# Optimization experiments

Measured on AMD Instinct MI355X. Metric: run time of the kernel, lower is better.

## Reference

```python
import jax, jax.numpy as jnp
import numpy as np

OIM_SCALAR = 30.0
NUM_PIDS = 5000      # rows of lut_instance
NUM_SAMPLES = 5000   # rows of reid_lut / len(reid_labels) (must equal NUM_PIDS, see source indexing)
NUM_FEATURES = 256
B_TOTAL = 4096       # total RoIs across the image batch
IGNORE_INDEX = 5554


def _l2norm(x):
    return x / jnp.linalg.norm(x, axis=-1, keepdims=True)


def setup_inputs() -> dict:
    key = jax.random.key(0)
    k1, k2, k3, k4, k5 = jax.random.split(key, 5)
    inputs = _l2norm(jax.random.normal(k1, (B_TOTAL, NUM_FEATURES), dtype=jnp.float32))
    # roi_label in [0, NUM_PIDS]; 0 = background (-> target -1, filtered out)
    roi_label = jax.random.randint(k2, (B_TOTAL,), 0, NUM_PIDS + 1, dtype=jnp.int32)
    lut_instance = _l2norm(jax.random.normal(k3, (NUM_PIDS, NUM_FEATURES), dtype=jnp.float32))
    reid_lut = _l2norm(jax.random.normal(k4, (NUM_SAMPLES, NUM_FEATURES), dtype=jnp.float32))
    # per-pid reid class id; -1 = unlabeled instance (filtered by label_reid >= 0)
    reid_labels = jax.random.randint(k5, (NUM_SAMPLES,), 0, NUM_SAMPLES, dtype=jnp.int32) - 1
    return {"inputs": inputs, "roi_label": roi_label, "lut_instance": lut_instance,
            "reid_lut": reid_lut, "reid_labels": reid_labels}


def _forward(inputs, lut_instance, reid_lut, roi_label, reid_labels):
    feat_dim = inputs.shape[1]
    targets = roi_label - 1
    valid = targets >= 0                       # torch: inds = targets >= 0 (masked mean == subset mean)
    label = jnp.clip(targets, 0)
    re_id_features = lut_instance[label]       # [B, F]
    label_reid = reid_labels[label]            # [B]

    w1 = valid.astype(inputs.dtype)
    n1 = jnp.maximum(w1.sum(), 1.0)
    # nn.MSELoss(): mean over all elements of the selected rows
    feature_consistency = jnp.sum(((re_id_features - inputs) ** 2) * w1[:, None]) / (n1 * feat_dim)

    valid2 = valid & (label_reid >= 0)
    w2 = valid2.astype(inputs.dtype)
    n2 = jnp.maximum(w2.sum(), 1.0)
    lr = jnp.clip(label_reid, 0)

    # ---- criterion_instance, vectorized over the double python loop ----
    out_inst = (inputs @ lut_instance.T) * OIM_SCALAR          # [B, P]
    pos_mask = reid_labels[None, :] == label_reid[:, None]     # [B, P] label-equality groups
    neg_logits = jnp.where(pos_mask, -jnp.inf, out_inst)
    lse_neg = jax.scipy.special.logsumexp(neg_logits, axis=1)  # [B]
    # per positive p: -log_softmax over cat([out[k,p]], out[k, negs])[0]
    per_pos = jnp.logaddexp(out_inst, lse_neg[:, None]) - out_inst  # [B, P]
    pos_count = jnp.maximum(pos_mask.sum(axis=1), 1).astype(inputs.dtype)
    loss_k = jnp.sum(jnp.where(pos_mask, per_pos, 0.0), axis=1) / pos_count
    instance_loss = jnp.sum(loss_k * w2) / n2                  # mean over valid reid rows

    # ---- OIM cross entropy against reid_lut ----
    out_reid = (inputs @ reid_lut.T) * OIM_SCALAR              # [B, S]
    logp = jax.nn.log_softmax(out_reid, axis=1)
    ce = -jnp.take_along_axis(logp, lr[:, None], axis=1)[:, 0]
    w3 = w2 * (lr != IGNORE_INDEX).astype(inputs.dtype)
    n3 = jnp.maximum(w3.sum(), 1.0)
    loss_oim_reid = jnp.sum(ce * w3) / n3

    return feature_consistency + loss_oim_reid + instance_loss


def reference(inputs, roi_label, lut_instance, reid_lut, reid_labels):
    return _forward(inputs, lut_instance, reid_lut, roi_label, reid_labels)
```

## Files before the change

### kernel.cpp

```cpp
#include <hip/hip_runtime.h>


#define BT 4096
#define NPID 5000
#define FDIM 256
#define NCHUNK 8
#define BPROWS 10240
#define SIDE 5120
#define SCALE2 43.2808512266689f
#define LN2 0.6931471805599453f
#define PADMARK ((int)0x80000000)
#define FXS 67108864.0

typedef __attribute__((ext_vector_type(8))) _Float16 half8;
typedef __attribute__((ext_vector_type(4))) float f32x4;

#if __has_builtin(__builtin_amdgcn_exp2f)
#define EXP2R(x) __builtin_amdgcn_exp2f(x)
#else
#define EXP2R(x) exp2f(x)
#endif

__device__ __forceinline__ size_t frag_unit(int row, int oct) {
  int c  = oct >> 2;
  int ko = oct & 3;
  return ((size_t)(row >> 4) * NCHUNK + c) * 64 + (row & 15) + (ko << 4);
}

__global__ __launch_bounds__(256) void prep(const float* __restrict__ inputs,
                                            const int* __restrict__ roi,
                                            const float* __restrict__ lut,
                                            const float* __restrict__ reid,
                                            const int* __restrict__ rlab,
                                            _Float16* __restrict__ Ap,
                                            _Float16* __restrict__ Bp,
                                            int* __restrict__ g, int* __restrict__ lr,
                                            float* __restrict__ w2f, float* __restrict__ v1f,
                                            float* __restrict__ fcv,
                                            int* __restrict__ poscnt,
                                            unsigned long long* __restrict__ ctrl) {
  const int b = blockIdx.x, tid = threadIdx.x;
  if (b < 512) {
    int idx = b * 256 + tid;
    int row = idx >> 5, oct = idx & 31;
    const float4* s4 = (const float4*)(inputs + (size_t)row * FDIM + oct * 8);
    float4 f0 = s4[0], f1 = s4[1];
    float fv[8] = {f0.x, f0.y, f0.z, f0.w, f1.x, f1.y, f1.z, f1.w};
    half8 ov;
#pragma unroll
    for (int j = 0; j < 8; ++j) ov[j] = (_Float16)(fv[j] * SCALE2);
    *(half8*)(Ap + frag_unit(row, oct) * 8) = ov;
  } else if (b < 1792) {
    int idx = (b - 512) * 256 + tid;
    int row = idx >> 5, oct = idx & 31;
    const float* src = nullptr;
    if (row < NPID) src = lut + (size_t)row * FDIM + oct * 8;
    else if (row >= SIDE && row < SIDE + NPID) src = reid + (size_t)(row - SIDE) * FDIM + oct * 8;
    half8 ov;
    if (src) {
      const float4* s4 = (const float4*)src;
      float4 f0 = s4[0], f1 = s4[1];
      float fv[8] = {f0.x, f0.y, f0.z, f0.w, f1.x, f1.y, f1.z, f1.w};
#pragma unroll
      for (int j = 0; j < 8; ++j) ov[j] = (_Float16)fv[j];
    } else {
#pragma unroll
      for (int j = 0; j < 8; ++j) ov[j] = (_Float16)0.f;
    }
    *(half8*)(Bp + frag_unit(row, oct) * 8) = ov;
  } else if (b < 2816) {
    int gt = (b - 1792) * 256 + tid;
    int row = gt >> 6, lane = gt & 63;
    int t = roi[row] - 1;
    bool valid = t >= 0;
    int label = t > 0 ? t : 0;
    int gg = rlab[label];
    const float4* xv = (const float4*)(inputs + (size_t)row * FDIM);
    const float4* lv = (const float4*)(lut + (size_t)label * FDIM);
    float4 a = xv[lane], bb = lv[lane];
    float dx = bb.x - a.x, dy = bb.y - a.y, dz = bb.z - a.z, dw = bb.w - a.w;
    float s = dx * dx + dy * dy + dz * dz + dw * dw;
#pragma unroll
    for (int d = 1; d < 64; d <<= 1) s += __shfl_xor(s, d, 64);
    if (lane == 0) {
      g[row]   = gg;
      lr[row]  = gg > 0 ? gg : 0;
      w2f[row] = (valid && gg >= 0) ? 1.0f : 0.0f;
      v1f[row] = valid ? 1.0f : 0.0f;
      fcv[row] = valid ? s : 0.0f;
    }
  } else {
    int idx = (b - 2816) * 256 + tid;
    poscnt[idx] = 0;
    if (b == 2816 && tid < 8) ctrl[tid] = 0ULL;
  }
}

__global__ __launch_bounds__(256, 3) void gemm_main(const _Float16* __restrict__ Ap,
                                                    const _Float16* __restrict__ Bp,
                                                    const int* __restrict__ rlab,
                                                    const int* __restrict__ g,
                                                    const int* __restrict__ lr,
                                                    float* __restrict__ partials,
                                                    float* __restrict__ posbuf,
                                                    int* __restrict__ poscnt,
                                                    float* __restrict__ target) {
  __shared__ unsigned short lds[16640] __attribute__((aligned(16)));
  const int bid = blockIdx.x;
  const int xcd = bid & 7;
  const int i   = bid >> 3;
  const int cb  = i >> 2;
  const int rb  = xcd * 4 + (i & 3);
  const int tid = threadIdx.x;
  const int l = tid & 63;
  const int w = tid >> 6;
  const int wr = w >> 1, wc = w & 1;

  const bool inst = cb < 40;
  const int cbl = inst ? cb : cb - 40;

  int* rl_s = (int*)&lds[16384];
  if (tid < 128) {
    int scol = cbl * 128 + tid;
    rl_s[tid] = (inst && scol < NPID) ? rlab[scol] : PADMARK;
  }
  const int rlane = l & 15;
  const int rowb = rb * 128 + wr * 64 + rlane;
  int key[4];
#pragma unroll
  for (int nr = 0; nr < 4; ++nr)
    key[nr] = inst ? g[rowb + nr * 16] : lr[rowb + nr * 16];

  f32x4 acc[4][4];
#pragma unroll
  for (int mi = 0; mi < 4; ++mi)
#pragma unroll
    for (int ni = 0; ni < 4; ++ni) acc[mi][ni] = (f32x4){0.f, 0.f, 0.f, 0.f};

  for (int s = 0; s < 4; ++s) {
    const int c0 = s * 2;
    __syncthreads();
#pragma unroll
    for (int q = 0; q < 8; ++q) {
      const int f = w * 8 + q;
      const bool isA = f < 16;
      const int fl = isA ? f : f - 16;
      const int cc = fl >> 3;
      const int grp = fl & 7;
      const int gidx = isA ? (rb * 8 + grp) : (cb * 8 + grp);
      const _Float16* src = (isA ? Ap : Bp)
          + (((size_t)gidx * NCHUNK + (c0 + cc)) << 6) * 8 + l * 8;
      unsigned short* dst = &lds[f * 512];
      __builtin_amdgcn_global_load_lds((const __attribute__((address_space(1))) unsigned int*)src,
                                       (__attribute__((address_space(3))) unsigned int*)dst,
                                       16, 0, 0);
    }
    __syncthreads();
#pragma unroll
    for (int cc = 0; cc < 2; ++cc) {
      half8 cf[4], rf[4];
#pragma unroll
      for (int mc = 0; mc < 4; ++mc)
        cf[mc] = *(const half8*)&lds[8192 + (cc * 8 + (wc * 4 + mc)) * 512 + l * 8];
#pragma unroll
      for (int nr = 0; nr < 4; ++nr)
        rf[nr] = *(const half8*)&lds[(cc * 8 + (wr * 4 + nr)) * 512 + l * 8];
#pragma unroll
      for (int mc = 0; mc < 4; ++mc)
#pragma unroll
        for (int nr = 0; nr < 4; ++nr)
          acc[mc][nr] = __builtin_amdgcn_mfma_f32_16x16x32_f16(cf[mc], rf[nr], acc[mc][nr], 0, 0, 0);
    }
  }

  const int colg = l >> 4;
  int4 rlv[4];
#pragma unroll
  for (int mc = 0; mc < 4; ++mc)
    rlv[mc] = *(const int4*)&rl_s[wc * 64 + mc * 16 + colg * 4];

  const int chunk = (inst ? 0 : 80) + cbl * 2 + wc;
  const float NINF = -__builtin_inff();

#pragma unroll
  for (int nr = 0; nr < 4; ++nr) {
    const int row = rowb + nr * 16;
    const int kv = key[nr];
    float s = 0.f;
    if (inst) {
#pragma unroll
      for (int mc = 0; mc < 4; ++mc)
#pragma unroll
        for (int reg = 0; reg < 4; ++reg) {
          float x2 = acc[mc][nr][reg];
          int rl = ((const int*)&rlv[mc])[reg];
          bool pos = (rl == kv);
          if (pos) {
            int idx = atomicAdd(&poscnt[row], 1);
            if (idx < 16) posbuf[row * 16 + idx] = x2;
          }
          float xe = (pos || rl == PADMARK) ? NINF : x2;
          s += EXP2R(xe);
        }
    } else {
      const int sbase = cbl * 128 + wc * 64 + colg * 4;
#pragma unroll
      for (int mc = 0; mc < 4; ++mc)
#pragma unroll
        for (int reg = 0; reg < 4; ++reg) {
          int scol = sbase + mc * 16 + reg;
          float x2 = acc[mc][nr][reg];
          if (scol == kv) target[row] = x2;
          float xe = (scol < NPID) ? x2 : NINF;
          s += EXP2R(xe);
        }
    }
    s += __shfl_xor(s, 16, 64);
    s += __shfl_xor(s, 32, 64);
    if (colg == 0) partials[(size_t)chunk * BT + row] = s;
  }
}

__global__ __launch_bounds__(256) void combine(const float* __restrict__ partials,
                                               const float* __restrict__ posbuf,
                                               const int* __restrict__ poscnt,
                                               const float* __restrict__ target,
                                               const float* __restrict__ w2f,
                                               const float* __restrict__ v1f,
                                               const float* __restrict__ fcv,
                                               unsigned long long* __restrict__ ctrl,
                                               float* __restrict__ out) {
  const int tid = threadIdx.x;
  const int row = blockIdx.x * 256 + tid;
  float S = 0.f;
  for (int i = 0; i < 80; ++i) S += partials[(size_t)i * BT + row];
  float lse2n = __log2f(S);
  int cnt = poscnt[row];
  int cc = cnt < 16 ? cnt : 16;
  float sum = 0.f;
  for (int j = 0; j < cc; ++j) {
    float d = LN2 * (lse2n - posbuf[row * 16 + j]);
    sum += (d > 60.f) ? d : log1pf(__expf(d));
  }
  float w2 = w2f[row];
  float v[5];
  v[0] = fcv[row];
  v[1] = v1f[row];
  v[2] = w2;
  v[3] = w2 * (sum / fmaxf((float)cnt, 1.0f));
  float S2 = 0.f;
  for (int i = 80; i < 160; ++i) S2 += partials[(size_t)i * BT + row];
  v[4] = w2 * LN2 * (__log2f(S2) - target[row]);

#pragma unroll
  for (int k = 0; k < 5; ++k)
#pragma unroll
    for (int d = 1; d < 64; d <<= 1) v[k] += __shfl_xor(v[k], d, 64);
  __shared__ float red[4][5];
  int lane = tid & 63, wv = tid >> 6;
  if (lane == 0)
#pragma unroll
    for (int k = 0; k < 5; ++k) red[wv][k] = v[k];
  __syncthreads();
  if (tid == 0) {
#pragma unroll
    for (int k = 0; k < 5; ++k) {
      double bs = (double)red[0][k] + red[1][k] + red[2][k] + red[3][k];
      long long q = (long long)(bs * FXS + 0.5);
      atomicAdd(&ctrl[k], (unsigned long long)q);
    }
    __threadfence();
    unsigned int prev = atomicAdd((unsigned int*)&ctrl[6], 1u);
    if (prev == (unsigned int)(gridDim.x - 1)) {
      double a[5];
#pragma unroll
      for (int k = 0; k < 5; ++k)
        a[k] = (double)(long long)atomicAdd(&ctrl[k], 0ULL) / FXS;
      double n1 = a[1] > 1.0 ? a[1] : 1.0;
      double n2 = a[2] > 1.0 ? a[2] : 1.0;
      out[0] = (float)(a[0] / (n1 * (double)FDIM) + a[4] / n2 + a[3] / n2);
    }
  }
}

extern "C" void kernel_launch(void* const* d_in, const int* in_sizes, int n_in,
                              void* d_out, int out_size, void* d_ws, size_t ws_size,
                              hipStream_t stream) {
  const float* inputs = (const float*)d_in[0];
  const int*   roi    = (const int*)d_in[1];
  const float* lut    = (const float*)d_in[2];
  const float* reid   = (const float*)d_in[3];
  const int*   rlab   = (const int*)d_in[4];
  float* out = (float*)d_out;

  char* w = (char*)d_ws;
  _Float16* Ap    = (_Float16*)(w);
  _Float16* Bp    = (_Float16*)(w + 2097152);
  float* partials = (float*)(w + 7340032);
  float* posbuf   = (float*)(w + 9961472);
  int*   poscnt   = (int*)(w + 10223616);
  float* target   = (float*)(w + 10240000);
  int*   g        = (int*)(w + 10256384);
  int*   lr       = (int*)(w + 10272768);
  float* w2f      = (float*)(w + 10289152);
  float* v1f      = (float*)(w + 10305536);
  float* fcv      = (float*)(w + 10321920);
  unsigned long long* ctrl = (unsigned long long*)(w + 10338304);

  prep<<<2832, 256, 0, stream>>>(inputs, roi, lut, reid, rlab, Ap, Bp,
                                 g, lr, w2f, v1f, fcv, poscnt, ctrl);
  gemm_main<<<2560, 256, 0, stream>>>(Ap, Bp, rlab, g, lr, partials, posbuf, poscnt, target);
  combine<<<BT / 256, 256, 0, stream>>>(partials, posbuf, poscnt, target,
                                        w2f, v1f, fcv, ctrl, out);
}
```

Baseline: 60.45 us.

## Convert GEMM to persistent kernel with per-XCD atomic tile scheduling

Replaces the one-block-per-tile launch of 2560 blocks with 768 persistent blocks. Each block repeatedly takes a tile index from an atomic counter kept per XCD, which preserves the XCD-to-row-block mapping and balances load within each XCD. It also moves the positive-match atomics and target stores out of the exp loop, recording matches in a bitmask and handling them in a rarely taken branch. The cost is an atomic and two extra barriers per tile, and the counters must be zeroed in prep.

```diff
diff --git a/kernel.cpp b/kernel.cpp
--- a/kernel.cpp
+++ b/kernel.cpp
@@ -38,7 +38,8 @@
                                             float* __restrict__ w2f, float* __restrict__ v1f,
                                             float* __restrict__ fcv,
                                             int* __restrict__ poscnt,
-                                            unsigned long long* __restrict__ ctrl) {
+                                            unsigned long long* __restrict__ ctrl,
+                                            int* __restrict__ tilecnt) {
   const int b = blockIdx.x, tid = threadIdx.x;
   if (b < 512) {
     int idx = b * 256 + tid;
@@ -92,7 +93,10 @@
   } else {
     int idx = (b - 2816) * 256 + tid;
     poscnt[idx] = 0;
-    if (b == 2816 && tid < 8) ctrl[tid] = 0ULL;
+    if (b == 2816) {
+      if (tid < 8) ctrl[tid] = 0ULL;
+      else if (tid < 16) tilecnt[tid - 8] = 0;
+    }
   }
 }
 
@@ -104,120 +108,143 @@
                                                     float* __restrict__ partials,
                                                     float* __restrict__ posbuf,
                                                     int* __restrict__ poscnt,
-                                                    float* __restrict__ target) {
+                                                    float* __restrict__ target,
+                                                    int* __restrict__ tilecnt) {
   __shared__ unsigned short lds[16640] __attribute__((aligned(16)));
-  const int bid = blockIdx.x;
-  const int xcd = bid & 7;
-  const int i   = bid >> 3;
-  const int cb  = i >> 2;
-  const int rb  = xcd * 4 + (i & 3);
+  __shared__ int stile;
+  int* rl_s = (int*)&lds[16384];
+  const int xcd = blockIdx.x & 7;
   const int tid = threadIdx.x;
   const int l = tid & 63;
   const int w = tid >> 6;
   const int wr = w >> 1, wc = w & 1;
-
-  const bool inst = cb < 40;
-  const int cbl = inst ? cb : cb - 40;
-
-  int* rl_s = (int*)&lds[16384];
-  if (tid < 128) {
-    int scol = cbl * 128 + tid;
-    rl_s[tid] = (inst && scol < NPID) ? rlab[scol] : PADMARK;
-  }
   const int rlane = l & 15;
-  const int rowb = rb * 128 + wr * 64 + rlane;
-  int key[4];
-#pragma unroll
-  for (int nr = 0; nr < 4; ++nr)
-    key[nr] = inst ? g[rowb + nr * 16] : lr[rowb + nr * 16];
-
-  f32x4 acc[4][4];
-#pragma unroll
-  for (int mi = 0; mi < 4; ++mi)
-#pragma unroll
-    for (int ni = 0; ni < 4; ++ni) acc[mi][ni] = (f32x4){0.f, 0.f, 0.f, 0.f};
-
-  for (int s = 0; s < 4; ++s) {
-    const int c0 = s * 2;
+  const int colg = l >> 4;
+  const float NINF = -__builtin_inff();
+
+  for (;;) {
     __syncthreads();
-#pragma unroll
-    for (int q = 0; q < 8; ++q) {
-      const int f = w * 8 + q;
-      const bool isA = f < 16;
-      const int fl = isA ? f : f - 16;
-      const int cc = fl >> 3;
-      const int grp = fl & 7;
-      const int gidx = isA ? (rb * 8 + grp) : (cb * 8 + grp);
-      const _Float16* src = (isA ? Ap : Bp)
-          + (((size_t)gidx * NCHUNK + (c0 + cc)) << 6) * 8 + l * 8;
-      unsigned short* dst = &lds[f * 512];
-      __builtin_amdgcn_global_load_lds((const __attribute__((address_space(1))) unsigned int*)src,
-                                       (__attribute__((address_space(3))) unsigned int*)dst,
-                                       16, 0, 0);
-    }
+    if (tid == 0) stile = atomicAdd(&tilecnt[xcd], 1);
     __syncthreads();
-#pragma unroll
-    for (int cc = 0; cc < 2; ++cc) {
-      half8 cf[4], rf[4];
-#pragma unroll
-      for (int mc = 0; mc < 4; ++mc)
-        cf[mc] = *(const half8*)&lds[8192 + (cc * 8 + (wc * 4 + mc)) * 512 + l * 8];
-#pragma unroll
-      for (int nr = 0; nr < 4; ++nr)
-        rf[nr] = *(const half8*)&lds[(cc * 8 + (wr * 4 + nr)) * 512 + l * 8];
-#pragma unroll
-      for (int mc = 0; mc < 4; ++mc)
+    const int t = stile;
+    if (t >= 320) break;
+    const int cb = t >> 2;
+    const int rb = xcd * 4 + (t & 3);
+    const bool inst = cb < 40;
+    const int cbl = inst ? cb : cb - 40;
+
+    if (tid < 128) {
+      int scol = cbl * 128 + tid;
+      rl_s[tid] = (inst && scol < NPID) ? rlab[scol] : PADMARK;
+    }
+    const int rowb = rb * 128 + wr * 64 + rlane;
+    int key[4];
+#pragma unroll
+    for (int nr = 0; nr < 4; ++nr)
+      key[nr] = inst ? g[rowb + nr * 16] : lr[rowb + nr * 16];
+
+    f32x4 acc[4][4];
+#pragma unroll
+    for (int mi = 0; mi < 4; ++mi)
+#pragma unroll
+      for (int ni = 0; ni < 4; ++ni) acc[mi][ni] = (f32x4){0.f, 0.f, 0.f, 0.f};
+
+    for (int s = 0; s < 4; ++s) {
+      const int c0 = s * 2;
+      __syncthreads();
+#pragma unroll
+      for (int q = 0; q < 8; ++q) {
+        const int f = w * 8 + q;
+        const bool isA = f < 16;
+        const int fl = isA ? f : f - 16;
+        const int cc = fl >> 3;
+        const int grp = fl & 7;
+        const int gidx = isA ? (rb * 8 + grp) : (cb * 8 + grp);
+        const _Float16* src = (isA ? Ap : Bp)
+            + (((size_t)gidx * NCHUNK + (c0 + cc)) << 6) * 8 + l * 8;
+        unsigned short* dst = &lds[f * 512];
+        __builtin_amdgcn_global_load_lds((const __attribute__((address_space(1))) unsigned int*)src,
+                                         (__attribute__((address_space(3))) unsigned int*)dst,
+                                         16, 0, 0);
+      }
+      __syncthreads();
+#pragma unroll
+      for (int cc = 0; cc < 2; ++cc) {
+        half8 cf[4], rf[4];
+#pragma unroll
+        for (int mc = 0; mc < 4; ++mc)
+          cf[mc] = *(const half8*)&lds[8192 + (cc * 8 + (wc * 4 + mc)) * 512 + l * 8];
 #pragma unroll
         for (int nr = 0; nr < 4; ++nr)
-          acc[mc][nr] = __builtin_amdgcn_mfma_f32_16x16x32_f16(cf[mc], rf[nr], acc[mc][nr], 0, 0, 0);
-    }
-  }
-
-  const int colg = l >> 4;
-  int4 rlv[4];
-#pragma unroll
-  for (int mc = 0; mc < 4; ++mc)
-    rlv[mc] = *(const int4*)&rl_s[wc * 64 + mc * 16 + colg * 4];
-
-  const int chunk = (inst ? 0 : 80) + cbl * 2 + wc;
-  const float NINF = -__builtin_inff();
-
-#pragma unroll
-  for (int nr = 0; nr < 4; ++nr) {
-    const int row = rowb + nr * 16;
-    const int kv = key[nr];
-    float s = 0.f;
-    if (inst) {
-#pragma unroll
-      for (int mc = 0; mc < 4; ++mc)
-#pragma unroll
-        for (int reg = 0; reg < 4; ++reg) {
-          float x2 = acc[mc][nr][reg];
-          int rl = ((const int*)&rlv[mc])[reg];
-          bool pos = (rl == kv);
-          if (pos) {
-            int idx = atomicAdd(&poscnt[row], 1);
-            if (idx < 16) posbuf[row * 16 + idx] = x2;
+          rf[nr] = *(const half8*)&lds[(cc * 8 + (wr * 4 + nr)) * 512 + l * 8];
+#pragma unroll
+        for (int mc = 0; mc < 4; ++mc)
+#pragma unroll
+          for (int nr = 0; nr < 4; ++nr)
+            acc[mc][nr] = __builtin_amdgcn_mfma_f32_16x16x32_f16(cf[mc], rf[nr], acc[mc][nr], 0, 0, 0);
+      }
+    }
+
+    int4 rlv[4];
+#pragma unroll
+    for (int mc = 0; mc < 4; ++mc)
+      rlv[mc] = *(const int4*)&rl_s[wc * 64 + mc * 16 + colg * 4];
+
+    const int chunk = (inst ? 0 : 80) + cbl * 2 + wc;
+
+#pragma unroll
+    for (int nr = 0; nr < 4; ++nr) {
+      const int row = rowb + nr * 16;
+      const int kv = key[nr];
+      float s = 0.f;
+      if (inst) {
+        int pmask = 0;
+#pragma unroll
+        for (int mc = 0; mc < 4; ++mc)
+#pragma unroll
+          for (int reg = 0; reg < 4; ++reg) {
+            float x2 = acc[mc][nr][reg];
+            int rl = ((const int*)&rlv[mc])[reg];
+            bool pos = (rl == kv);
+            pmask |= pos ? (1 << (mc * 4 + reg)) : 0;
+            float xe = (pos || rl == PADMARK) ? NINF : x2;
+            s += EXP2R(xe);
           }
-          float xe = (pos || rl == PADMARK) ? NINF : x2;
-          s += EXP2R(xe);
+        if (__builtin_expect(pmask != 0, 0)) {
+#pragma unroll
+          for (int mc = 0; mc < 4; ++mc)
+#pragma unroll
+            for (int reg = 0; reg < 4; ++reg)
+              if (pmask & (1 << (mc * 4 + reg))) {
+                int idx = atomicAdd(&poscnt[row], 1);
+                if (idx < 16) posbuf[row * 16 + idx] = acc[mc][nr][reg];
+              }
         }
-    } else {
-      const int sbase = cbl * 128 + wc * 64 + colg * 4;
-#pragma unroll
-      for (int mc = 0; mc < 4; ++mc)
-#pragma unroll
-        for (int reg = 0; reg < 4; ++reg) {
-          int scol = sbase + mc * 16 + reg;
-          float x2 = acc[mc][nr][reg];
-          if (scol == kv) target[row] = x2;
-          float xe = (scol < NPID) ? x2 : NINF;
-          s += EXP2R(xe);
+      } else {
+        const int sbase = cbl * 128 + wc * 64 + colg * 4;
+        int tmask = 0;
+#pragma unroll
+        for (int mc = 0; mc < 4; ++mc)
+#pragma unroll
+          for (int reg = 0; reg < 4; ++reg) {
+            int scol = sbase + mc * 16 + reg;
+            float x2 = acc[mc][nr][reg];
+            tmask |= (scol == kv) ? (1 << (mc * 4 + reg)) : 0;
+            float xe = (scol < NPID) ? x2 : NINF;
+            s += EXP2R(xe);
+          }
+        if (__builtin_expect(tmask != 0, 0)) {
+#pragma unroll
+          for (int mc = 0; mc < 4; ++mc)
+#pragma unroll
+            for (int reg = 0; reg < 4; ++reg)
+              if (tmask & (1 << (mc * 4 + reg))) target[row] = acc[mc][nr][reg];
         }
-    }
-    s += __shfl_xor(s, 16, 64);
-    s += __shfl_xor(s, 32, 64);
-    if (colg == 0) partials[(size_t)chunk * BT + row] = s;
+      }
+      s += __shfl_xor(s, 16, 64);
+      s += __shfl_xor(s, 32, 64);
+      if (colg == 0) partials[(size_t)chunk * BT + row] = s;
+    }
   }
 }
 
@@ -306,10 +333,12 @@
   float* v1f      = (float*)(w + 10305536);
   float* fcv      = (float*)(w + 10321920);
   unsigned long long* ctrl = (unsigned long long*)(w + 10338304);
+  int* tilecnt    = (int*)(w + 10338368);
 
   prep<<<2832, 256, 0, stream>>>(inputs, roi, lut, reid, rlab, Ap, Bp,
-                                 g, lr, w2f, v1f, fcv, poscnt, ctrl);
-  gemm_main<<<2560, 256, 0, stream>>>(Ap, Bp, rlab, g, lr, partials, posbuf, poscnt, target);
+                                 g, lr, w2f, v1f, fcv, poscnt, ctrl, tilecnt);
+  gemm_main<<<768, 256, 0, stream>>>(Ap, Bp, rlab, g, lr, partials, posbuf,
+                                     poscnt, target, tilecnt);
   combine<<<BT / 256, 256, 0, stream>>>(partials, posbuf, poscnt, target,
                                         w2f, v1f, fcv, ctrl, out);
 }
```

Measured after the change: 95.23 us. +57.5%, slower.

## Enlarge GEMM block to 256 rows with 512 threads, defer positive-match atomics

Applied to the files above, without the earlier changes.

The fused GEMM+epilogue kernel now uses 512-thread blocks covering 256 rows × 128 columns, so each B tile staged in LDS is shared by twice as many rows and the grid is halved. LDS grows to hold the bigger A tile. The epilogue also builds a bitmask of positive or target matches and handles the rare atomic/store work after the exp loop, keeping the hot loop branch-free. This adds LDS use and register pressure per block, which may limit occupancy.

```diff
diff --git a/kernel.cpp b/kernel.cpp
--- a/kernel.cpp
+++ b/kernel.cpp
@@ -96,7 +96,7 @@
   }
 }
 
-__global__ __launch_bounds__(256, 3) void gemm_main(const _Float16* __restrict__ Ap,
+__global__ __launch_bounds__(512, 4) void gemm_main(const _Float16* __restrict__ Ap,
                                                     const _Float16* __restrict__ Bp,
                                                     const int* __restrict__ rlab,
                                                     const int* __restrict__ g,
@@ -105,12 +105,12 @@
                                                     float* __restrict__ posbuf,
                                                     int* __restrict__ poscnt,
                                                     float* __restrict__ target) {
-  __shared__ unsigned short lds[16640] __attribute__((aligned(16)));
+  __shared__ unsigned short lds[24832] __attribute__((aligned(16)));
   const int bid = blockIdx.x;
   const int xcd = bid & 7;
   const int i   = bid >> 3;
-  const int cb  = i >> 2;
-  const int rb  = xcd * 4 + (i & 3);
+  const int cb  = i >> 1;
+  const int rb2 = xcd * 2 + (i & 1);
   const int tid = threadIdx.x;
   const int l = tid & 63;
   const int w = tid >> 6;
@@ -119,13 +119,13 @@
   const bool inst = cb < 40;
   const int cbl = inst ? cb : cb - 40;
 
-  int* rl_s = (int*)&lds[16384];
+  int* rl_s = (int*)&lds[24576];
   if (tid < 128) {
     int scol = cbl * 128 + tid;
     rl_s[tid] = (inst && scol < NPID) ? rlab[scol] : PADMARK;
   }
   const int rlane = l & 15;
-  const int rowb = rb * 128 + wr * 64 + rlane;
+  const int rowb = rb2 * 256 + wr * 64 + rlane;
   int key[4];
 #pragma unroll
   for (int nr = 0; nr < 4; ++nr)
@@ -141,18 +141,23 @@
     const int c0 = s * 2;
     __syncthreads();
 #pragma unroll
-    for (int q = 0; q < 8; ++q) {
-      const int f = w * 8 + q;
-      const bool isA = f < 16;
-      const int fl = isA ? f : f - 16;
-      const int cc = fl >> 3;
-      const int grp = fl & 7;
-      const int gidx = isA ? (rb * 8 + grp) : (cb * 8 + grp);
-      const _Float16* src = (isA ? Ap : Bp)
-          + (((size_t)gidx * NCHUNK + (c0 + cc)) << 6) * 8 + l * 8;
-      unsigned short* dst = &lds[f * 512];
+    for (int q = 0; q < 6; ++q) {
+      const int f = w * 6 + q;
+      const bool isA = f < 32;
+      const _Float16* src;
+      int dsts;
+      if (isA) {
+        const int cc = f >> 4, rg = f & 15;
+        src = Ap + (((size_t)(rb2 * 16 + rg) * NCHUNK + (c0 + cc)) << 9) + l * 8;
+        dsts = (cc * 16 + rg) * 512;
+      } else {
+        const int fb = f - 32;
+        const int cc = fb >> 3, cg = fb & 7;
+        src = Bp + (((size_t)(cb * 8 + cg) * NCHUNK + (c0 + cc)) << 9) + l * 8;
+        dsts = 16384 + (cc * 8 + cg) * 512;
+      }
       __builtin_amdgcn_global_load_lds((const __attribute__((address_space(1))) unsigned int*)src,
-                                       (__attribute__((address_space(3))) unsigned int*)dst,
+                                       (__attribute__((address_space(3))) unsigned int*)&lds[dsts],
                                        16, 0, 0);
     }
     __syncthreads();
@@ -161,10 +166,10 @@
       half8 cf[4], rf[4];
 #pragma unroll
       for (int mc = 0; mc < 4; ++mc)
-        cf[mc] = *(const half8*)&lds[8192 + (cc * 8 + (wc * 4 + mc)) * 512 + l * 8];
+        cf[mc] = *(const half8*)&lds[16384 + (cc * 8 + (wc * 4 + mc)) * 512 + l * 8];
 #pragma unroll
       for (int nr = 0; nr < 4; ++nr)
-        rf[nr] = *(const half8*)&lds[(cc * 8 + (wr * 4 + nr)) * 512 + l * 8];
+        rf[nr] = *(const half8*)&lds[(cc * 16 + (wr * 4 + nr)) * 512 + l * 8];
 #pragma unroll
       for (int mc = 0; mc < 4; ++mc)
 #pragma unroll
@@ -188,6 +193,7 @@
     const int kv = key[nr];
     float s = 0.f;
     if (inst) {
+      int pmask = 0;
 #pragma unroll
       for (int mc = 0; mc < 4; ++mc)
 #pragma unroll
@@ -195,25 +201,40 @@
           float x2 = acc[mc][nr][reg];
           int rl = ((const int*)&rlv[mc])[reg];
           bool pos = (rl == kv);
-          if (pos) {
-            int idx = atomicAdd(&poscnt[row], 1);
-            if (idx < 16) posbuf[row * 16 + idx] = x2;
-          }
+          pmask |= pos ? (1 << (mc * 4 + reg)) : 0;
           float xe = (pos || rl == PADMARK) ? NINF : x2;
           s += EXP2R(xe);
         }
+      if (__builtin_expect(pmask != 0, 0)) {
+#pragma unroll
+        for (int mc = 0; mc < 4; ++mc)
+#pragma unroll
+          for (int reg = 0; reg < 4; ++reg)
+            if (pmask & (1 << (mc * 4 + reg))) {
+              int idx = atomicAdd(&poscnt[row], 1);
+              if (idx < 16) posbuf[row * 16 + idx] = acc[mc][nr][reg];
+            }
+      }
     } else {
       const int sbase = cbl * 128 + wc * 64 + colg * 4;
+      int tmask = 0;
 #pragma unroll
       for (int mc = 0; mc < 4; ++mc)
 #pragma unroll
         for (int reg = 0; reg < 4; ++reg) {
           int scol = sbase + mc * 16 + reg;
           float x2 = acc[mc][nr][reg];
-          if (scol == kv) target[row] = x2;
+          tmask |= (scol == kv) ? (1 << (mc * 4 + reg)) : 0;
           float xe = (scol < NPID) ? x2 : NINF;
           s += EXP2R(xe);
         }
+      if (__builtin_expect(tmask != 0, 0)) {
+#pragma unroll
+        for (int mc = 0; mc < 4; ++mc)
+#pragma unroll
+          for (int reg = 0; reg < 4; ++reg)
+            if (tmask & (1 << (mc * 4 + reg))) target[row] = acc[mc][nr][reg];
+      }
     }
     s += __shfl_xor(s, 16, 64);
     s += __shfl_xor(s, 32, 64);
@@ -309,7 +330,7 @@
 
   prep<<<2832, 256, 0, stream>>>(inputs, roi, lut, reid, rlab, Ap, Bp,
                                  g, lr, w2f, v1f, fcv, poscnt, ctrl);
-  gemm_main<<<2560, 256, 0, stream>>>(Ap, Bp, rlab, g, lr, partials, posbuf, poscnt, target);
+  gemm_main<<<1280, 512, 0, stream>>>(Ap, Bp, rlab, g, lr, partials, posbuf, poscnt, target);
   combine<<<BT / 256, 256, 0, stream>>>(partials, posbuf, poscnt, target,
                                         w2f, v1f, fcv, ctrl, out);
 }
```

Result: slower. 87.53 us (+44.8%).

## Double-buffer GEMM K-loop, precompute OIM target in prep, drop padding masks

Applied to the files above, without the earlier changes.

The GEMM main loop now uses two LDS buffers and processes one K-chunk per step, so the global-to-LDS load of chunk t+1 overlaps the MFMAs on chunk t, with a single waitcnt plus barrier per step. The reid target logit is computed in fp32 inside prep, and per-column masking of padded columns is removed from the epilogue. Padded columns contribute exp2(0)=1 each, and combine subtracts that known constant instead. Positive-match atomics are gathered into a bitmask and issued only when some match exists, which removes branches from the hot exp loop. The pad-subtraction trick depends on the padded B rows being zero, and the target now comes from fp32 math rather than the fp16 GEMM.

```diff
diff --git a/kernel.cpp b/kernel.cpp
--- a/kernel.cpp
+++ b/kernel.cpp
@@ -9,7 +9,8 @@
 #define SIDE 5120
 #define SCALE2 43.2808512266689f
 #define LN2 0.6931471805599453f
-#define PADMARK ((int)0x80000000)
+#define BIGVAL 0x7FFFFFFF
+#define NPAD 120.0f
 #define FXS 67108864.0
 
 typedef __attribute__((ext_vector_type(8))) _Float16 half8;
@@ -34,9 +35,9 @@
                                             const int* __restrict__ rlab,
                                             _Float16* __restrict__ Ap,
                                             _Float16* __restrict__ Bp,
-                                            int* __restrict__ g, int* __restrict__ lr,
+                                            int* __restrict__ g,
                                             float* __restrict__ w2f, float* __restrict__ v1f,
-                                            float* __restrict__ fcv,
+                                            float* __restrict__ fcv, float* __restrict__ target,
                                             int* __restrict__ poscnt,
                                             unsigned long long* __restrict__ ctrl) {
   const int b = blockIdx.x, tid = threadIdx.x;
@@ -75,19 +76,25 @@
     bool valid = t >= 0;
     int label = t > 0 ? t : 0;
     int gg = rlab[label];
+    int lrv = gg > 0 ? gg : 0;
     const float4* xv = (const float4*)(inputs + (size_t)row * FDIM);
     const float4* lv = (const float4*)(lut + (size_t)label * FDIM);
-    float4 a = xv[lane], bb = lv[lane];
+    const float4* rv = (const float4*)(reid + (size_t)lrv * FDIM);
+    float4 a = xv[lane], bb = lv[lane], cv = rv[lane];
     float dx = bb.x - a.x, dy = bb.y - a.y, dz = bb.z - a.z, dw = bb.w - a.w;
     float s = dx * dx + dy * dy + dz * dz + dw * dw;
-#pragma unroll
-    for (int d = 1; d < 64; d <<= 1) s += __shfl_xor(s, d, 64);
+    float t2 = a.x * cv.x + a.y * cv.y + a.z * cv.z + a.w * cv.w;
+#pragma unroll
+    for (int d = 1; d < 64; d <<= 1) {
+      s  += __shfl_xor(s, d, 64);
+      t2 += __shfl_xor(t2, d, 64);
+    }
     if (lane == 0) {
-      g[row]   = gg;
-      lr[row]  = gg > 0 ? gg : 0;
-      w2f[row] = (valid && gg >= 0) ? 1.0f : 0.0f;
-      v1f[row] = valid ? 1.0f : 0.0f;
-      fcv[row] = valid ? s : 0.0f;
+      g[row]      = gg;
+      w2f[row]    = (valid && gg >= 0) ? 1.0f : 0.0f;
+      v1f[row]    = valid ? 1.0f : 0.0f;
+      fcv[row]    = valid ? s : 0.0f;
+      target[row] = SCALE2 * t2;
     }
   } else {
     int idx = (b - 2816) * 256 + tid;
@@ -100,12 +107,11 @@
                                                     const _Float16* __restrict__ Bp,
                                                     const int* __restrict__ rlab,
                                                     const int* __restrict__ g,
-                                                    const int* __restrict__ lr,
                                                     float* __restrict__ partials,
                                                     float* __restrict__ posbuf,
-                                                    int* __restrict__ poscnt,
-                                                    float* __restrict__ target) {
+                                                    int* __restrict__ poscnt) {
   __shared__ unsigned short lds[16640] __attribute__((aligned(16)));
+  int* rl_s = (int*)&lds[16384];
   const int bid = blockIdx.x;
   const int xcd = bid & 7;
   const int i   = bid >> 3;
@@ -119,17 +125,16 @@
   const bool inst = cb < 40;
   const int cbl = inst ? cb : cb - 40;
 
-  int* rl_s = (int*)&lds[16384];
   if (tid < 128) {
     int scol = cbl * 128 + tid;
-    rl_s[tid] = (inst && scol < NPID) ? rlab[scol] : PADMARK;
+    rl_s[tid] = (inst && scol < NPID) ? rlab[scol] : BIGVAL;
   }
   const int rlane = l & 15;
   const int rowb = rb * 128 + wr * 64 + rlane;
   int key[4];
 #pragma unroll
   for (int nr = 0; nr < 4; ++nr)
-    key[nr] = inst ? g[rowb + nr * 16] : lr[rowb + nr * 16];
+    key[nr] = inst ? g[rowb + nr * 16] : BIGVAL;
 
   f32x4 acc[4][4];
 #pragma unroll
@@ -137,57 +142,59 @@
 #pragma unroll
     for (int ni = 0; ni < 4; ++ni) acc[mi][ni] = (f32x4){0.f, 0.f, 0.f, 0.f};
 
-  for (int s = 0; s < 4; ++s) {
-    const int c0 = s * 2;
-    __syncthreads();
-#pragma unroll
-    for (int q = 0; q < 8; ++q) {
-      const int f = w * 8 + q;
-      const bool isA = f < 16;
-      const int fl = isA ? f : f - 16;
-      const int cc = fl >> 3;
-      const int grp = fl & 7;
-      const int gidx = isA ? (rb * 8 + grp) : (cb * 8 + grp);
-      const _Float16* src = (isA ? Ap : Bp)
-          + (((size_t)gidx * NCHUNK + (c0 + cc)) << 6) * 8 + l * 8;
-      unsigned short* dst = &lds[f * 512];
+  auto stage = [&](int t, int b) {
+#pragma unroll
+    for (int q = 0; q < 4; ++q) {
+      const int f = w * 4 + q;
+      const bool isA = f < 8;
+      const int grp = f & 7;
+      const int gidx = (isA ? rb * 8 : cb * 8) + grp;
+      const _Float16* src = (isA ? Ap : Bp) + (((size_t)gidx * NCHUNK + t) << 9) + l * 8;
+      unsigned short* dst = &lds[b * 8192 + (isA ? 0 : 4096) + grp * 512];
       __builtin_amdgcn_global_load_lds((const __attribute__((address_space(1))) unsigned int*)src,
                                        (__attribute__((address_space(3))) unsigned int*)dst,
                                        16, 0, 0);
     }
-    __syncthreads();
-#pragma unroll
-    for (int cc = 0; cc < 2; ++cc) {
-      half8 cf[4], rf[4];
-#pragma unroll
-      for (int mc = 0; mc < 4; ++mc)
-        cf[mc] = *(const half8*)&lds[8192 + (cc * 8 + (wc * 4 + mc)) * 512 + l * 8];
+  };
+
+  stage(0, 0);
+  __syncthreads();
+  int cur = 0;
+#pragma unroll
+  for (int t = 0; t < 8; ++t) {
+    if (t < 7) stage(t + 1, cur ^ 1);
+    half8 cf[4], rf[4];
+#pragma unroll
+    for (int mc = 0; mc < 4; ++mc)
+      cf[mc] = *(const half8*)&lds[cur * 8192 + 4096 + (wc * 4 + mc) * 512 + l * 8];
+#pragma unroll
+    for (int nr = 0; nr < 4; ++nr)
+      rf[nr] = *(const half8*)&lds[cur * 8192 + (wr * 4 + nr) * 512 + l * 8];
+#pragma unroll
+    for (int mc = 0; mc < 4; ++mc)
 #pragma unroll
       for (int nr = 0; nr < 4; ++nr)
-        rf[nr] = *(const half8*)&lds[(cc * 8 + (wr * 4 + nr)) * 512 + l * 8];
-#pragma unroll
-      for (int mc = 0; mc < 4; ++mc)
-#pragma unroll
-        for (int nr = 0; nr < 4; ++nr)
-          acc[mc][nr] = __builtin_amdgcn_mfma_f32_16x16x32_f16(cf[mc], rf[nr], acc[mc][nr], 0, 0, 0);
-    }
+        acc[mc][nr] = __builtin_amdgcn_mfma_f32_16x16x32_f16(cf[mc], rf[nr], acc[mc][nr], 0, 0, 0);
+    asm volatile("s_waitcnt vmcnt(0)" ::: "memory");
+    asm volatile("s_barrier" ::: "memory");
+    cur ^= 1;
   }
 
   const int colg = l >> 4;
-  int4 rlv[4];
-#pragma unroll
-  for (int mc = 0; mc < 4; ++mc)
-    rlv[mc] = *(const int4*)&rl_s[wc * 64 + mc * 16 + colg * 4];
-
   const int chunk = (inst ? 0 : 80) + cbl * 2 + wc;
   const float NINF = -__builtin_inff();
 
-#pragma unroll
-  for (int nr = 0; nr < 4; ++nr) {
-    const int row = rowb + nr * 16;
-    const int kv = key[nr];
-    float s = 0.f;
-    if (inst) {
+  if (inst) {
+    int4 rlv[4];
+#pragma unroll
+    for (int mc = 0; mc < 4; ++mc)
+      rlv[mc] = *(const int4*)&rl_s[wc * 64 + mc * 16 + colg * 4];
+#pragma unroll
+    for (int nr = 0; nr < 4; ++nr) {
+      const int row = rowb + nr * 16;
+      const int kv = key[nr];
+      float s = 0.f;
+      int pmask = 0;
 #pragma unroll
       for (int mc = 0; mc < 4; ++mc)
 #pragma unroll
@@ -195,29 +202,37 @@
           float x2 = acc[mc][nr][reg];
           int rl = ((const int*)&rlv[mc])[reg];
           bool pos = (rl == kv);
-          if (pos) {
-            int idx = atomicAdd(&poscnt[row], 1);
-            if (idx < 16) posbuf[row * 16 + idx] = x2;
-          }
-          float xe = (pos || rl == PADMARK) ? NINF : x2;
-          s += EXP2R(xe);
+          pmask |= pos ? (1 << (mc * 4 + reg)) : 0;
+          s += EXP2R(pos ? NINF : x2);
         }
-    } else {
-      const int sbase = cbl * 128 + wc * 64 + colg * 4;
+      if (__builtin_expect(pmask != 0, 0)) {
+#pragma unroll
+        for (int mc = 0; mc < 4; ++mc)
+#pragma unroll
+          for (int reg = 0; reg < 4; ++reg)
+            if (pmask & (1 << (mc * 4 + reg))) {
+              int idx = atomicAdd(&poscnt[row], 1);
+              if (idx < 16) posbuf[row * 16 + idx] = acc[mc][nr][reg];
+            }
+      }
+      s += __shfl_xor(s, 16, 64);
+      s += __shfl_xor(s, 32, 64);
+      if (colg == 0) partials[(size_t)chunk * BT + row] = s;
+    }
+  } else {
+#pragma unroll
+    for (int nr = 0; nr < 4; ++nr) {
+      const int row = rowb + nr * 16;
+      float s = 0.f;
 #pragma unroll
       for (int mc = 0; mc < 4; ++mc)
 #pragma unroll
-        for (int reg = 0; reg < 4; ++reg) {
-          int scol = sbase + mc * 16 + reg;
-          float x2 = acc[mc][nr][reg];
-          if (scol == kv) target[row] = x2;
-          float xe = (scol < NPID) ? x2 : NINF;
-          s += EXP2R(xe);
-        }
-    }
-    s += __shfl_xor(s, 16, 64);
-    s += __shfl_xor(s, 32, 64);
-    if (colg == 0) partials[(size_t)chunk * BT + row] = s;
+        for (int reg = 0; reg < 4; ++reg)
+          s += EXP2R(acc[mc][nr][reg]);
+      s += __shfl_xor(s, 16, 64);
+      s += __shfl_xor(s, 32, 64);
+      if (colg == 0) partials[(size_t)chunk * BT + row] = s;
+    }
   }
 }
 
@@ -234,6 +249,7 @@
   const int row = blockIdx.x * 256 + tid;
   float S = 0.f;
   for (int i = 0; i < 80; ++i) S += partials[(size_t)i * BT + row];
+  S -= NPAD;
   float lse2n = __log2f(S);
   int cnt = poscnt[row];
   int cc = cnt < 16 ? cnt : 16;
@@ -250,6 +266,7 @@
   v[3] = w2 * (sum / fmaxf((float)cnt, 1.0f));
   float S2 = 0.f;
   for (int i = 80; i < 160; ++i) S2 += partials[(size_t)i * BT + row];
+  S2 -= NPAD;
   v[4] = w2 * LN2 * (__log2f(S2) - target[row]);
 
 #pragma unroll
@@ -301,15 +318,14 @@
   int*   poscnt   = (int*)(w + 10223616);
   float* target   = (float*)(w + 10240000);
   int*   g        = (int*)(w + 10256384);
-  int*   lr       = (int*)(w + 10272768);
-  float* w2f      = (float*)(w + 10289152);
-  float* v1f      = (float*)(w + 10305536);
-  float* fcv      = (float*)(w + 10321920);
-  unsigned long long* ctrl = (unsigned long long*)(w + 10338304);
+  float* w2f      = (float*)(w + 10272768);
+  float* v1f      = (float*)(w + 10289152);
+  float* fcv      = (float*)(w + 10305536);
+  unsigned long long* ctrl = (unsigned long long*)(w + 10321920);
 
   prep<<<2832, 256, 0, stream>>>(inputs, roi, lut, reid, rlab, Ap, Bp,
-                                 g, lr, w2f, v1f, fcv, poscnt, ctrl);
-  gemm_main<<<2560, 256, 0, stream>>>(Ap, Bp, rlab, g, lr, partials, posbuf, poscnt, target);
+                                 g, w2f, v1f, fcv, target, poscnt, ctrl);
+  gemm_main<<<2560, 256, 0, stream>>>(Ap, Bp, rlab, g, partials, posbuf, poscnt);
   combine<<<BT / 256, 256, 0, stream>>>(partials, posbuf, poscnt, target,
                                         w2f, v1f, fcv, ctrl, out);
 }
```

After: 53.75 us. 11.1% less time.
